# Optimization experiments

Measured on AMD Instinct MI355X. Metric: run time of the kernel, lower is better.

The kernel has to match this reference:

```python
import jax, jax.numpy as jnp
import numpy as np
from jax import lax

SIGMA_S = 60.0
SIGMA_R = 0.4
ITER_NUM = 2
SQRT2 = 1.4142135623730951
SQRT3 = 1.7320508075688772


def _linrec_op(l, r):
    # combine two affine maps x -> a*x + b applied in sequence (l first, then r)
    al, bl = l
    ar, br = r
    return (al * ar, ar * bl + br)


def _recursive_filter(img, D, sigma):
    """Domain-transform recursive filter along the last axis (width).
    Forward pass:  x_i = V_i * x_{i-1} + (1 - V_i) * img_i,  x_0 = img_0
    Backward pass: y_i = V_{i+1} * y_{i+1} + (1 - V_{i+1}) * x_i, y_{w-1} = x_{w-1}
    img: [B,C,H,W], D: [B,1,H,W]
    """
    a = jnp.exp(jnp.float32(-SQRT2 / sigma))
    V = jnp.broadcast_to(a ** D, img.shape)  # [B,C,H,W]

    # left-to-right linear recurrence via parallel associative scan
    af = V.at[..., 0].set(0.0)  # x_0 = img_0
    bf = (1.0 - af) * img
    _, x = lax.associative_scan(_linrec_op, (af, bf), axis=-1)

    # right-to-left pass: coefficient at position i is V[i+1]; flip, scan, flip back
    ab = jnp.concatenate([V[..., 1:], jnp.zeros_like(V[..., :1])], axis=-1)
    ab = ab[..., ::-1]
    bb = (1.0 - ab) * x[..., ::-1]
    _, y = lax.associative_scan(_linrec_op, (ab, bb), axis=-1)
    return y[..., ::-1]


def setup_inputs() -> dict:
    key = jax.random.key(0)
    k1, k2 = jax.random.split(key)
    img = jax.random.normal(k1, (4, 32, 512, 512), dtype=jnp.float32)
    edge = jax.random.uniform(k2, (4, 1, 512, 512), dtype=jnp.float32)
    return {"img": img, "edge": edge}


def reference(img, edge):
    dHdx = 1.0 + (SIGMA_S / SIGMA_R) * edge            # [B,1,H,W]
    dVdy = jnp.swapaxes(dHdx, 2, 3)                    # [B,1,W,H]
    denom = float(np.sqrt(4.0 ** ITER_NUM - 1.0))
    for i in range(ITER_NUM):
        sigma_i = SIGMA_S * SQRT3 * (2.0 ** (ITER_NUM - (i + 1))) / denom
        img = _recursive_filter(img, dHdx, sigma_i)    # filter along W
        img = jnp.swapaxes(img, 2, 3)
        img = _recursive_filter(img, dVdy, sigma_i)    # filter along H
        img = jnp.swapaxes(img, 2, 3)
    return img
```

## Files before the change

### kernel.cpp

```cpp
#include <hip/hip_runtime.h>

#define C0F (-0.026352313834736496f)
#define C1F (-0.052704627669472993f)

#define NB 4
#define NC 32
#define NH 512
#define NW 512

typedef _Float16 h16;
typedef __attribute__((ext_vector_type(8))) _Float16 f16x8;

__device__ __forceinline__ void load8(const float* p, float* x) {
    float4 a = *reinterpret_cast<const float4*>(p);
    float4 b = *reinterpret_cast<const float4*>(p + 4);
    x[0]=a.x; x[1]=a.y; x[2]=a.z; x[3]=a.w;
    x[4]=b.x; x[5]=b.y; x[6]=b.z; x[7]=b.w;
}
__device__ __forceinline__ void load8(const h16* p, float* x) {
    f16x8 h = *reinterpret_cast<const f16x8*>(p);
    #pragma unroll
    for (int i = 0; i < 8; ++i) x[i] = (float)h[i];
}
__device__ __forceinline__ void store8(float* p, const float* x) {
    *reinterpret_cast<float4*>(p)     = make_float4(x[0],x[1],x[2],x[3]);
    *reinterpret_cast<float4*>(p + 4) = make_float4(x[4],x[5],x[6],x[7]);
}
__device__ __forceinline__ void store8(h16* p, const float* x) {
    f16x8 h;
    #pragma unroll
    for (int i = 0; i < 8; ++i) h[i] = (h16)x[i];
    *reinterpret_cast<f16x8*>(p) = h;
}

__global__ __launch_bounds__(256) void vtab_kernel(const float* __restrict__ edge,
                                                   float* __restrict__ v0,
                                                   float* __restrict__ v1) {
    int i = blockIdx.x * 256 + threadIdx.x;
    float4 e = reinterpret_cast<const float4*>(edge)[i];
    float dx = 1.f + 150.f * e.x;
    float dy = 1.f + 150.f * e.y;
    float dz = 1.f + 150.f * e.z;
    float dw = 1.f + 150.f * e.w;
    float4 a0, a1;
    a0.x = expf(C0F * dx); a0.y = expf(C0F * dy); a0.z = expf(C0F * dz); a0.w = expf(C0F * dw);
    a1.x = expf(C1F * dx); a1.y = expf(C1F * dy); a1.z = expf(C1F * dz); a1.w = expf(C1F * dw);
    reinterpret_cast<float4*>(v0)[i] = a0;
    reinterpret_cast<float4*>(v1)[i] = a1;
}

template <typename ST, typename DT>
__global__ __launch_bounds__(256) void hpass_kernel(const ST* __restrict__ src,
                                                    DT* __restrict__ dst,
                                                    const float* __restrict__ vt) {
    const int lane = threadIdx.x & 63;
    const int wv   = threadIdx.x >> 6;
    const int row  = (blockIdx.x << 2) + wv;
    const int h    = row & (NH - 1);
    const int bc   = row >> 9;
    const int b    = bc >> 5;
    const ST* srow = src + ((size_t)row << 9);
    DT*       drow = dst + ((size_t)row << 9);
    const float* vrow = vt + (((size_t)(b << 9) + h) << 9);
    const int g0 = lane << 3;

    float x[8], v[8];
    load8(srow + g0, x);
    load8(vrow + g0, v);

    float A = 1.f, Bv = 0.f;
    #pragma unroll
    for (int i = 0; i < 8; ++i) {
        float a = v[i];
        if (lane == 0 && i == 0) a = 0.f;
        Bv = a * Bv + (1.f - a) * x[i];
        A  = a * A;
    }
    #pragma unroll
    for (int d = 1; d < 64; d <<= 1) {
        float Ap = __shfl_up(A, d);
        float Bp = __shfl_up(Bv, d);
        if (lane >= d) { Bv = A * Bp + Bv; A = A * Ap; }
    }
    float carry = __shfl_up(Bv, 1);
    if (lane == 0) carry = 0.f;
    float xp = carry;
    #pragma unroll
    for (int i = 0; i < 8; ++i) {
        float a = v[i];
        if (lane == 0 && i == 0) a = 0.f;
        xp = a * xp + (1.f - a) * x[i];
        x[i] = xp;
    }

    float vn = __shfl_down(v[0], 1);
    float A2 = 1.f, B2 = 0.f;
    #pragma unroll
    for (int i = 7; i >= 0; --i) {
        float a = (i < 7) ? v[i + 1] : ((lane == 63) ? 0.f : vn);
        B2 = a * B2 + (1.f - a) * x[i];
        A2 = a * A2;
    }
    #pragma unroll
    for (int d = 1; d < 64; d <<= 1) {
        float Ap = __shfl_down(A2, d);
        float Bp = __shfl_down(B2, d);
        if (lane < 64 - d) { B2 = A2 * Bp + B2; A2 = A2 * Ap; }
    }
    float cb = __shfl_down(B2, 1);
    if (lane == 63) cb = 0.f;
    float yn = cb;
    #pragma unroll
    for (int i = 7; i >= 0; --i) {
        float a = (i < 7) ? v[i + 1] : ((lane == 63) ? 0.f : vn);
        yn = a * yn + (1.f - a) * x[i];
        x[i] = yn;
    }

    store8(drow + g0, x);
}

#define VROWS 32
template <typename ST, typename DT>
__global__ __launch_bounds__(512) void vpass_kernel(const ST* __restrict__ src,
                                                    DT* __restrict__ dst,
                                                    const float* __restrict__ vt) {
    const int col   = threadIdx.x & 31;
    const int hc    = threadIdx.x >> 5;
    const int strip = blockIdx.x & 15;
    const int bc    = blockIdx.x >> 4;
    const int b     = bc >> 5;
    const int w     = (strip << 5) + col;
    const ST*    sbase = src + ((size_t)bc << 18) + w;
    DT*          dbase = dst + ((size_t)bc << 18) + w;
    const float* vb    = vt  + ((size_t)b  << 18) + w;
    const int h0 = hc << 5;

    float x[VROWS], v[VROWS];
    #pragma unroll
    for (int i = 0; i < VROWS; ++i) x[i] = (float)sbase[(size_t)(h0 + i) << 9];
    #pragma unroll
    for (int i = 0; i < VROWS; ++i) v[i] = vb[(size_t)(h0 + i) << 9];

    __shared__ float sA[16][32], sB[16][32], sC[16][32], sV[16][32];

    float A = 1.f, Bv = 0.f;
    #pragma unroll
    for (int i = 0; i < VROWS; ++i) {
        float a = v[i];
        if (hc == 0 && i == 0) a = 0.f;
        Bv = a * Bv + (1.f - a) * x[i];
        A  = a * A;
    }
    sA[hc][col] = A; sB[hc][col] = Bv;
    __syncthreads();
    if (hc == 0) {
        float c = 0.f;
        #pragma unroll
        for (int k = 0; k < 16; ++k) {
            float a_ = sA[k][col], b_ = sB[k][col];
            sC[k][col] = c;
            c = a_ * c + b_;
        }
    }
    __syncthreads();
    float xp = sC[hc][col];
    #pragma unroll
    for (int i = 0; i < VROWS; ++i) {
        float a = v[i];
        if (hc == 0 && i == 0) a = 0.f;
        xp = a * xp + (1.f - a) * x[i];
        x[i] = xp;
    }
    sV[hc][col] = v[0];
    __syncthreads();
    float vnext = (hc < 15) ? sV[hc + 1][col] : 0.f;

    A = 1.f; Bv = 0.f;
    #pragma unroll
    for (int i = VROWS - 1; i >= 0; --i) {
        float a = (i < VROWS - 1) ? v[i + 1] : ((hc == 15) ? 0.f : vnext);
        Bv = a * Bv + (1.f - a) * x[i];
        A  = a * A;
    }
    sA[hc][col] = A; sB[hc][col] = Bv;
    __syncthreads();
    if (hc == 0) {
        float c = 0.f;
        #pragma unroll
        for (int k = 15; k >= 0; --k) {
            float a_ = sA[k][col], b_ = sB[k][col];
            sC[k][col] = c;
            c = a_ * c + b_;
        }
    }
    __syncthreads();
    float yn = sC[hc][col];
    #pragma unroll
    for (int i = VROWS - 1; i >= 0; --i) {
        float a = (i < VROWS - 1) ? v[i + 1] : ((hc == 15) ? 0.f : vnext);
        yn = a * yn + (1.f - a) * x[i];
        x[i] = yn;
    }
    #pragma unroll
    for (int i = 0; i < VROWS; ++i) dbase[(size_t)(h0 + i) << 9] = (DT)x[i];
}

extern "C" void kernel_launch(void* const* d_in, const int* in_sizes, int n_in,
                              void* d_out, int out_size, void* d_ws, size_t ws_size,
                              hipStream_t stream) {
    const float* img  = (const float*)d_in[0];
    const float* edge = (const float*)d_in[1];
    float* out = (float*)d_out;

    const size_t NBHW  = (size_t)NB * NH * NW;
    const size_t NTOT  = (size_t)NB * NC * NH * NW;
    float* v0 = (float*)d_ws;
    float* v1 = v0 + NBHW;
    h16*   tmp = (h16*)(v1 + NBHW);
    const size_t need = NBHW * 8 + NTOT * 2;

    vtab_kernel<<<(int)(NBHW / (256 * 4)), 256, 0, stream>>>(edge, v0, v1);

    const int HG = NB * NC * NH / 4;
    const int VG = NB * NC * (NW / 32);

    if (ws_size >= need) {
        hpass_kernel<float, h16><<<HG, 256, 0, stream>>>(img, tmp, v0);
        vpass_kernel<h16, h16><<<VG, 512, 0, stream>>>(tmp, tmp, v0);
        hpass_kernel<h16, h16><<<HG, 256, 0, stream>>>(tmp, tmp, v1);
        vpass_kernel<h16, float><<<VG, 512, 0, stream>>>(tmp, out, v1);
    } else {
        hpass_kernel<float, float><<<HG, 256, 0, stream>>>(img, out, v0);
        vpass_kernel<float, float><<<VG, 512, 0, stream>>>(out, out, v0);
        hpass_kernel<float, float><<<HG, 256, 0, stream>>>(out, out, v1);
        vpass_kernel<float, float><<<VG, 512, 0, stream>>>(out, out, v1);
    }
}
```

Baseline: 186.6 us.

## Replace vertical passes with row-scan plus shared-memory transpose passes

Measured after the change: 160.8 us. 1.16x faster.

```diff
diff --git a/kernel.cpp b/kernel.cpp
--- a/kernel.cpp
+++ b/kernel.cpp
@@ -31,6 +31,143 @@
     #pragma unroll
     for (int i = 0; i < 8; ++i) h[i] = (h16)x[i];
     *reinterpret_cast<f16x8*>(p) = h;
+}
+
+__device__ __forceinline__ void row_scan(float (&x)[8], const float (&v)[8], int lane) {
+    float A = 1.f, Bv = 0.f;
+    #pragma unroll
+    for (int i = 0; i < 8; ++i) {
+        float a = v[i];
+        if (lane == 0 && i == 0) a = 0.f;
+        Bv = a * Bv + (1.f - a) * x[i];
+        A *= a;
+    }
+    #pragma unroll
+    for (int d = 1; d < 64; d <<= 1) {
+        float Ap = __shfl_up(A, d);
+        float Bp = __shfl_up(Bv, d);
+        if (lane >= d) { Bv = A * Bp + Bv; A *= Ap; }
+    }
+    float carry = __shfl_up(Bv, 1);
+    if (lane == 0) carry = 0.f;
+    float xp = carry;
+    #pragma unroll
+    for (int i = 0; i < 8; ++i) {
+        float a = v[i];
+        if (lane == 0 && i == 0) a = 0.f;
+        xp = a * xp + (1.f - a) * x[i];
+        x[i] = xp;
+    }
+    float vn = __shfl_down(v[0], 1);
+    float A2 = 1.f, B2 = 0.f;
+    #pragma unroll
+    for (int i = 7; i >= 0; --i) {
+        float a = (i < 7) ? v[i + 1] : ((lane == 63) ? 0.f : vn);
+        B2 = a * B2 + (1.f - a) * x[i];
+        A2 *= a;
+    }
+    #pragma unroll
+    for (int d = 1; d < 64; d <<= 1) {
+        float Ap = __shfl_down(A2, d);
+        float Bp = __shfl_down(B2, d);
+        if (lane < 64 - d) { B2 = A2 * Bp + B2; A2 *= Ap; }
+    }
+    float cb = __shfl_down(B2, 1);
+    if (lane == 63) cb = 0.f;
+    float yn = cb;
+    #pragma unroll
+    for (int i = 7; i >= 0; --i) {
+        float a = (i < 7) ? v[i + 1] : ((lane == 63) ? 0.f : vn);
+        yn = a * yn + (1.f - a) * x[i];
+        x[i] = yn;
+    }
+}
+
+__global__ __launch_bounds__(256) void vtab_t_kernel(const float* __restrict__ edge,
+                                                     float* __restrict__ v0,
+                                                     float* __restrict__ v1,
+                                                     float* __restrict__ v0t,
+                                                     float* __restrict__ v1t) {
+    __shared__ float T0[64][65], T1[64][65];
+    const int t  = threadIdx.x;
+    const int i  = t & 15;
+    const int q  = t >> 4;
+    const int b  = blockIdx.x >> 6;
+    const int tt = blockIdx.x & 63;
+    const int h0 = (tt >> 3) << 6;
+    const int w0 = (tt & 7) << 6;
+    const size_t ib = (size_t)b << 18;
+    #pragma unroll
+    for (int rr = 0; rr < 4; ++rr) {
+        const int r = q + (rr << 4);
+        const size_t off = ib + ((size_t)(h0 + r) << 9) + w0 + (i << 2);
+        float4 e = *reinterpret_cast<const float4*>(edge + off);
+        float4 a0, a1; float d;
+        d = 1.f + 150.f * e.x; a0.x = expf(C0F*d); a1.x = expf(C1F*d);
+        d = 1.f + 150.f * e.y; a0.y = expf(C0F*d); a1.y = expf(C1F*d);
+        d = 1.f + 150.f * e.z; a0.z = expf(C0F*d); a1.z = expf(C1F*d);
+        d = 1.f + 150.f * e.w; a0.w = expf(C0F*d); a1.w = expf(C1F*d);
+        *reinterpret_cast<float4*>(v0 + off) = a0;
+        *reinterpret_cast<float4*>(v1 + off) = a1;
+        const int c = i << 2;
+        T0[r][c+0]=a0.x; T0[r][c+1]=a0.y; T0[r][c+2]=a0.z; T0[r][c+3]=a0.w;
+        T1[r][c+0]=a1.x; T1[r][c+1]=a1.y; T1[r][c+2]=a1.z; T1[r][c+3]=a1.w;
+    }
+    __syncthreads();
+    #pragma unroll
+    for (int rr = 0; rr < 4; ++rr) {
+        const int w = q + (rr << 4);
+        const int c = i << 2;
+        float4 o0, o1;
+        o0.x=T0[c+0][w]; o0.y=T0[c+1][w]; o0.z=T0[c+2][w]; o0.w=T0[c+3][w];
+        o1.x=T1[c+0][w]; o1.y=T1[c+1][w]; o1.z=T1[c+2][w]; o1.w=T1[c+3][w];
+        const size_t off = ib + ((size_t)(w0 + w) << 9) + h0 + c;
+        *reinterpret_cast<float4*>(v0t + off) = o0;
+        *reinterpret_cast<float4*>(v1t + off) = o1;
+    }
+}
+
+template <typename ST, typename DT>
+__global__ __launch_bounds__(512) void rs_pass(const ST* __restrict__ src,
+                                               DT* __restrict__ dst,
+                                               const float* __restrict__ vt) {
+    __shared__ h16 tile[64 * 512];
+    const int lane = threadIdx.x & 63;
+    const int wv   = threadIdx.x >> 6;
+    const int bc   = blockIdx.x >> 3;
+    const int b    = bc >> 5;
+    const int rho0 = (blockIdx.x & 7) << 6;
+    const ST*    sb = src + ((size_t)bc << 18);
+    const float* vb = vt  + ((size_t)b  << 18);
+
+    #pragma unroll
+    for (int k = 0; k < 8; ++k) {
+        const int r   = (wv << 3) + k;
+        const int row = rho0 + r;
+        float x[8], v[8];
+        load8(sb + ((size_t)row << 9) + (lane << 3), x);
+        load8(vb + ((size_t)row << 9) + (lane << 3), v);
+        row_scan(x, v, lane);
+        f16x8 hx;
+        #pragma unroll
+        for (int i = 0; i < 8; ++i) hx[i] = (h16)x[i];
+        const int cc = (((lane + wv) & 63) << 3);
+        *reinterpret_cast<f16x8*>(&tile[r * 512 + cc]) = hx;
+    }
+    __syncthreads();
+    const int g = lane >> 3;
+    const int j = lane & 7;
+    #pragma unroll
+    for (int m = 0; m < 8; ++m) {
+        const int c = (wv << 6) + (m << 3) + g;
+        float y[8];
+        #pragma unroll
+        for (int k = 0; k < 8; ++k) {
+            const int rr = (j << 3) + k;
+            y[k] = (float)tile[rr * 512 + ((c + (j << 3)) & 511)];
+        }
+        store8(dst + ((size_t)bc << 18) + ((size_t)c << 9) + rho0 + (j << 3), y);
+    }
 }
 
 __global__ __launch_bounds__(256) void vtab_kernel(const float* __restrict__ edge,
@@ -63,60 +200,10 @@
     DT*       drow = dst + ((size_t)row << 9);
     const float* vrow = vt + (((size_t)(b << 9) + h) << 9);
     const int g0 = lane << 3;
-
     float x[8], v[8];
     load8(srow + g0, x);
     load8(vrow + g0, v);
-
-    float A = 1.f, Bv = 0.f;
-    #pragma unroll
-    for (int i = 0; i < 8; ++i) {
-        float a = v[i];
-        if (lane == 0 && i == 0) a = 0.f;
-        Bv = a * Bv + (1.f - a) * x[i];
-        A  = a * A;
-    }
-    #pragma unroll
-    for (int d = 1; d < 64; d <<= 1) {
-        float Ap = __shfl_up(A, d);
-        float Bp = __shfl_up(Bv, d);
-        if (lane >= d) { Bv = A * Bp + Bv; A = A * Ap; }
-    }
-    float carry = __shfl_up(Bv, 1);
-    if (lane == 0) carry = 0.f;
-    float xp = carry;
-    #pragma unroll
-    for (int i = 0; i < 8; ++i) {
-        float a = v[i];
-        if (lane == 0 && i == 0) a = 0.f;
-        xp = a * xp + (1.f - a) * x[i];
-        x[i] = xp;
-    }
-
-    float vn = __shfl_down(v[0], 1);
-    float A2 = 1.f, B2 = 0.f;
-    #pragma unroll
-    for (int i = 7; i >= 0; --i) {
-        float a = (i < 7) ? v[i + 1] : ((lane == 63) ? 0.f : vn);
-        B2 = a * B2 + (1.f - a) * x[i];
-        A2 = a * A2;
-    }
-    #pragma unroll
-    for (int d = 1; d < 64; d <<= 1) {
-        float Ap = __shfl_down(A2, d);
-        float Bp = __shfl_down(B2, d);
-        if (lane < 64 - d) { B2 = A2 * Bp + B2; A2 = A2 * Ap; }
-    }
-    float cb = __shfl_down(B2, 1);
-    if (lane == 63) cb = 0.f;
-    float yn = cb;
-    #pragma unroll
-    for (int i = 7; i >= 0; --i) {
-        float a = (i < 7) ? v[i + 1] : ((lane == 63) ? 0.f : vn);
-        yn = a * yn + (1.f - a) * x[i];
-        x[i] = yn;
-    }
-
+    row_scan(x, v, lane);
     store8(drow + g0, x);
 }
 
@@ -135,32 +222,29 @@
     DT*          dbase = dst + ((size_t)bc << 18) + w;
     const float* vb    = vt  + ((size_t)b  << 18) + w;
     const int h0 = hc << 5;
-
     float x[VROWS], v[VROWS];
     #pragma unroll
     for (int i = 0; i < VROWS; ++i) x[i] = (float)sbase[(size_t)(h0 + i) << 9];
     #pragma unroll
     for (int i = 0; i < VROWS; ++i) v[i] = vb[(size_t)(h0 + i) << 9];
-
     __shared__ float sA[16][32], sB[16][32], sC[16][32], sV[16][32];
-
     float A = 1.f, Bv = 0.f;
     #pragma unroll
     for (int i = 0; i < VROWS; ++i) {
         float a = v[i];
         if (hc == 0 && i == 0) a = 0.f;
         Bv = a * Bv + (1.f - a) * x[i];
-        A  = a * A;
+        A *= a;
     }
     sA[hc][col] = A; sB[hc][col] = Bv;
     __syncthreads();
     if (hc == 0) {
-        float c = 0.f;
+        float cr = 0.f;
         #pragma unroll
         for (int k = 0; k < 16; ++k) {
             float a_ = sA[k][col], b_ = sB[k][col];
-            sC[k][col] = c;
-            c = a_ * c + b_;
+            sC[k][col] = cr;
+            cr = a_ * cr + b_;
         }
     }
     __syncthreads();
@@ -175,23 +259,22 @@
     sV[hc][col] = v[0];
     __syncthreads();
     float vnext = (hc < 15) ? sV[hc + 1][col] : 0.f;
-
     A = 1.f; Bv = 0.f;
     #pragma unroll
     for (int i = VROWS - 1; i >= 0; --i) {
         float a = (i < VROWS - 1) ? v[i + 1] : ((hc == 15) ? 0.f : vnext);
         Bv = a * Bv + (1.f - a) * x[i];
-        A  = a * A;
+        A *= a;
     }
     sA[hc][col] = A; sB[hc][col] = Bv;
     __syncthreads();
     if (hc == 0) {
-        float c = 0.f;
+        float cr = 0.f;
         #pragma unroll
         for (int k = 15; k >= 0; --k) {
             float a_ = sA[k][col], b_ = sB[k][col];
-            sC[k][col] = c;
-            c = a_ * c + b_;
+            sC[k][col] = cr;
+            cr = a_ * cr + b_;
         }
     }
     __syncthreads();
@@ -213,24 +296,37 @@
     const float* edge = (const float*)d_in[1];
     float* out = (float*)d_out;
 
-    const size_t NBHW  = (size_t)NB * NH * NW;
-    const size_t NTOT  = (size_t)NB * NC * NH * NW;
-    float* v0 = (float*)d_ws;
-    float* v1 = v0 + NBHW;
-    h16*   tmp = (h16*)(v1 + NBHW);
-    const size_t need = NBHW * 8 + NTOT * 2;
-
-    vtab_kernel<<<(int)(NBHW / (256 * 4)), 256, 0, stream>>>(edge, v0, v1);
-
-    const int HG = NB * NC * NH / 4;
-    const int VG = NB * NC * (NW / 32);
-
-    if (ws_size >= need) {
+    const size_t NBHW = (size_t)NB * NH * NW;
+    const size_t NTOT = (size_t)NB * NC * NH * NW;
+    float* v0  = (float*)d_ws;
+    float* v1  = v0  + NBHW;
+    float* v0t = v1  + NBHW;
+    float* v1t = v0t + NBHW;
+    h16*   tA  = (h16*)(v1t + NBHW);
+    h16*   tB  = (h16*)d_out;
+    const size_t needNew = NBHW * 16 + NTOT * 2;
+    const size_t needT2  = NBHW * 8  + NTOT * 2;
+
+    if (ws_size >= needNew) {
+        vtab_t_kernel<<<NB * 64, 256, 0, stream>>>(edge, v0, v1, v0t, v1t);
+        const int G = NB * NC * 8;
+        rs_pass<float, h16><<<G, 512, 0, stream>>>(img, tA, v0);
+        rs_pass<h16,  h16><<<G, 512, 0, stream>>>(tA, tB, v0t);
+        rs_pass<h16,  h16><<<G, 512, 0, stream>>>(tB, tA, v1);
+        rs_pass<h16, float><<<G, 512, 0, stream>>>(tA, out, v1t);
+    } else if (ws_size >= needT2) {
+        h16* tmp = (h16*)(v0t);
+        vtab_kernel<<<(int)(NBHW / (256 * 4)), 256, 0, stream>>>(edge, v0, v1);
+        const int HG = NB * NC * NH / 4;
+        const int VG = NB * NC * (NW / 32);
         hpass_kernel<float, h16><<<HG, 256, 0, stream>>>(img, tmp, v0);
         vpass_kernel<h16, h16><<<VG, 512, 0, stream>>>(tmp, tmp, v0);
         hpass_kernel<h16, h16><<<HG, 256, 0, stream>>>(tmp, tmp, v1);
         vpass_kernel<h16, float><<<VG, 512, 0, stream>>>(tmp, out, v1);
     } else {
+        vtab_kernel<<<(int)(NBHW / (256 * 4)), 256, 0, stream>>>(edge, v0, v1);
+        const int HG = NB * NC * NH / 4;
+        const int VG = NB * NC * (NW / 32);
         hpass_kernel<float, float><<<HG, 256, 0, stream>>>(img, out, v0);
         vpass_kernel<float, float><<<VG, 512, 0, stream>>>(out, out, v0);
         hpass_kernel<float, float><<<HG, 256, 0, stream>>>(out, out, v1);
```
